# Optimization experiments

Measured on AMD Instinct MI355X. Metric: run time of the kernel, lower is better.

The kernel has to match this reference:

```python
import jax, jax.numpy as jnp
import numpy as np

B, C, L = 32, 64, 4096
PS, STRIDE = 16, 8
PC = (L - PS) // STRIDE + 1  # 511
HID = 64


def setup_inputs() -> dict:
    key = jax.random.key(0)
    k = jax.random.split(key, 5)
    X = jax.random.normal(k[0], (B, C, L), dtype=jnp.float32)
    W1 = jax.random.normal(k[1], (HID, PS), dtype=jnp.float32) * 0.05  # Conv1d(1,64,PS) weight
    b1 = jax.random.normal(k[2], (HID,), dtype=jnp.float32) * 0.05
    W2 = jax.random.normal(k[3], (2, HID), dtype=jnp.float32) * 0.05   # Conv1d(64,2,1) weight
    b2 = jax.random.normal(k[4], (2,), dtype=jnp.float32) * 0.05
    return {"X": X, "W1": W1, "b1": b1, "W2": W2, "b2": b2}


def reference(X, W1, b1, W2, b2):
    Bn, Cn, Ln = X.shape
    s_bias = (PS - 1) / 2.0
    # anchors: center of each patch along the sequence axis
    anchor = jnp.arange(PC, dtype=X.dtype) * STRIDE + 0.5 * (PS - 1)  # (PC,)

    # ---- OffsetPredictor: unfold into (B, C, PC, PS) sliding windows ----
    idx = jnp.arange(PC)[:, None] * STRIDE + jnp.arange(PS)[None, :]  # (PC, PS)
    patches = X[:, :, idx]  # (B, C, PC, PS)
    # Conv1d(1, HID, PS) over a length-PS window == dense matmul with W1
    h = jax.nn.gelu(jnp.einsum('bcps,ks->bcpk', patches, W1) + b1, approximate=False)
    off = jnp.einsum('bcpk,jk->bcpj', h, W2) + b2  # (B, C, PC, 2)
    off = off.transpose(0, 2, 1, 3)  # (B, PC, C, 2)

    # ---- BoxCoder.decode ----
    dx = off[..., 0]
    ds = jax.nn.relu(off[..., 1] + s_bias)
    ref = anchor[None, :, None]
    lo = jnp.clip((dx + ref - ds) / (Ln - 1), 0.0, 1.0)  # (B, PC, C)
    hi = jnp.clip((dx + ref + ds) / (Ln - 1), 0.0, 1.0)

    # ---- BoxCoder.meshgrid: linear interp from box endpoints (align_corners) ----
    t = jnp.arange(PS, dtype=X.dtype) / (PS - 1)  # (PS,)
    xs = lo[..., None] + (hi - lo)[..., None] * t  # (B, PC, C, PS), in [0,1]
    ys = jnp.arange(Cn, dtype=X.dtype) / (Cn - 1)  # (C,), in [0,1]

    # ---- grid_sample(img=(B,1,C,L), grid=(xs,ys)*2-1, bilinear, align_corners=True) ----
    ix = xs * (Ln - 1)                                            # (B, PC, C, PS)
    iy = jnp.broadcast_to(ys[None, None, :, None] * (Cn - 1), ix.shape)
    ix0 = jnp.floor(ix)
    iy0 = jnp.floor(iy)
    wx = ix - ix0
    wy = iy - iy0
    ix0i = jnp.clip(ix0.astype(jnp.int32), 0, Ln - 1)
    ix1i = jnp.clip(ix0i + 1, 0, Ln - 1)
    iy0i = jnp.clip(iy0.astype(jnp.int32), 0, Cn - 1)
    iy1i = jnp.clip(iy0i + 1, 0, Cn - 1)

    gather = jax.vmap(lambda x, r, c: x[r, c])  # over batch; x:(C,L)
    v00 = gather(X, iy0i, ix0i)
    v01 = gather(X, iy0i, ix1i)
    v10 = gather(X, iy1i, ix0i)
    v11 = gather(X, iy1i, ix1i)
    out = (v00 * (1 - wx) + v01 * wx) * (1 - wy) + (v10 * (1 - wx) + v11 * wx) * wy
    # (B, PC, C, PS) -> (B, C, PC, PS)
    return out.transpose(0, 2, 1, 3)
```

## Files before the change

### kernel.cpp

```cpp
#include <hip/hip_runtime.h>
#include <math.h>

#define B_    32
#define C_    64
#define L_    4096
#define PS_   16
#define STR_  8
#define PC_   511
#define HID_  64

__global__ __launch_bounds__(256) void depatch_kernel(
    const float* __restrict__ X,
    const float* __restrict__ W1,
    const float* __restrict__ b1,
    const float* __restrict__ W2,
    const float* __restrict__ b2,
    float* __restrict__ out)
{
    __shared__ float s_row[L_];
    __shared__ float s_W1[HID_ * PS_];
    __shared__ float s_b1[HID_];
    __shared__ float s_W2[2 * HID_];
    __shared__ float s_b2[2];

    const int tid = threadIdx.x;
    const int bc  = blockIdx.x;
    const float* xrow = X + (size_t)bc * L_;

    {
        const float4* src4 = reinterpret_cast<const float4*>(xrow);
        float4* dst4 = reinterpret_cast<float4*>(s_row);
        #pragma unroll
        for (int i = 0; i < 4; ++i) dst4[tid + 256 * i] = src4[tid + 256 * i];

        reinterpret_cast<float4*>(s_W1)[tid] =
            reinterpret_cast<const float4*>(W1)[tid];
        if (tid < 16)
            reinterpret_cast<float4*>(s_b1)[tid] =
                reinterpret_cast<const float4*>(b1)[tid];
        if (tid < 32)
            reinterpret_cast<float4*>(s_W2)[tid] =
                reinterpret_cast<const float4*>(W2)[tid];
        if (tid < 2) s_b2[tid] = b2[tid];
    }
    __syncthreads();

    const float bias0 = s_b2[0];
    const float bias1 = s_b2[1];

    for (int p = tid; p < PC_; p += 256) {
        float pt[PS_];
        {
            const float4* prow = reinterpret_cast<const float4*>(s_row + p * STR_);
            #pragma unroll
            for (int i = 0; i < 4; ++i) {
                float4 v = prow[i];
                pt[4*i + 0] = v.x; pt[4*i + 1] = v.y;
                pt[4*i + 2] = v.z; pt[4*i + 3] = v.w;
            }
        }

        float dx  = bias0;
        float dsv = bias1;
        #pragma unroll 8
        for (int k = 0; k < HID_; ++k) {
            float acc = s_b1[k];
            const float* w = s_W1 + k * PS_;
            #pragma unroll
            for (int s = 0; s < PS_; ++s) acc = fmaf(pt[s], w[s], acc);
            float g = 0.5f * acc * (1.0f + erff(acc * 0.70710678118654752440f));
            dx  = fmaf(g, s_W2[k],        dx);
            dsv = fmaf(g, s_W2[HID_ + k], dsv);
        }

        const float refp = (float)(p * STR_) + 7.5f;
        const float ds2  = fmaxf(dsv + 7.5f, 0.0f);
        float lo = (dx + refp - ds2) / 4095.0f;
        float hi = (dx + refp + ds2) / 4095.0f;
        lo = fminf(fmaxf(lo, 0.0f), 1.0f);
        hi = fminf(fmaxf(hi, 0.0f), 1.0f);
        const float span = hi - lo;

        float outv[PS_];
        #pragma unroll
        for (int s = 0; s < PS_; ++s) {
            float t  = (float)s / 15.0f;
            float xs = lo + span * t;
            float ix = xs * 4095.0f;
            float ix0f = floorf(ix);
            float wx = ix - ix0f;
            int ix0 = (int)ix0f;
            ix0 = min(max(ix0, 0), L_ - 1);
            int ix1 = min(ix0 + 1, L_ - 1);
            float v0 = s_row[ix0];
            float v1 = s_row[ix1];
            outv[s] = v0 * (1.0f - wx) + v1 * wx;
        }

        float4* o4 = reinterpret_cast<float4*>(out + ((size_t)bc * PC_ + p) * PS_);
        #pragma unroll
        for (int i = 0; i < 4; ++i) {
            float4 v;
            v.x = outv[4*i + 0]; v.y = outv[4*i + 1];
            v.z = outv[4*i + 2]; v.w = outv[4*i + 3];
            o4[i] = v;
        }
    }
}

extern "C" void kernel_launch(void* const* d_in, const int* in_sizes, int n_in,
                              void* d_out, int out_size, void* d_ws, size_t ws_size,
                              hipStream_t stream) {
    const float* X  = (const float*)d_in[0];
    const float* W1 = (const float*)d_in[1];
    const float* b1 = (const float*)d_in[2];
    const float* W2 = (const float*)d_in[3];
    const float* b2 = (const float*)d_in[4];
    float* out = (float*)d_out;

    dim3 grid(B_ * C_);
    dim3 block(256);
    depatch_kernel<<<grid, block, 0, stream>>>(X, W1, b1, W2, b2, out);
}
```

Before: 148.0 us.

## Use fast GELU approximation and process two patches per thread with global weights

Replaces the exact erff-based GELU with an Abramowitz-Stegun polynomial erf approximation built on the hardware reciprocal and exp2. Each thread now handles two patches at once, sharing each weight load across both accumulators, and reads the weights directly from global memory (uniform, scalar-cacheable) instead of staging them in shared memory. The sampling math is simplified by working in index space. The erf approximation has an error around 1e-7 relative, which may shift sampling positions slightly.

```diff
diff --git a/kernel.cpp b/kernel.cpp
--- a/kernel.cpp
+++ b/kernel.cpp
@@ -1,13 +1,57 @@
 #include <hip/hip_runtime.h>
 #include <math.h>
 
-#define B_    32
-#define C_    64
 #define L_    4096
 #define PS_   16
 #define STR_  8
 #define PC_   511
 #define HID_  64
+#define NBLK_ 2048
+
+__device__ __forceinline__ float gelu_as(float x) {
+    float az = fabsf(x) * 0.70710678118654752440f;
+    float d  = fmaf(0.3275911f, az, 1.0f);
+    float t  = __builtin_amdgcn_rcpf(d);
+    float p  = fmaf(1.061405429f, t, -1.453152027f);
+    p = fmaf(p, t, 1.421413741f);
+    p = fmaf(p, t, -0.284496736f);
+    p = fmaf(p, t, 0.254829592f);
+    p = p * t;
+    float e  = __builtin_amdgcn_exp2f(az * az * -1.4426950408889634f);
+    float r  = fmaf(-p, e, 1.0f);
+    r = copysignf(r, x);
+    float h = 0.5f * x;
+    return fmaf(h, r, h);
+}
+
+__device__ __forceinline__ void sample_store(const float* __restrict__ s_row,
+                                             float* __restrict__ outp,
+                                             int p, float dx, float ds) {
+    const float refp = (float)(p * STR_) + 7.5f;
+    const float d2   = fmaxf(ds + 7.5f, 0.0f);
+    const float a    = dx + refp;
+    const float loi  = fminf(fmaxf(a - d2, 0.0f), 4095.0f);
+    const float hii  = fminf(fmaxf(a + d2, 0.0f), 4095.0f);
+    const float span = hii - loi;
+
+    float4 o[4];
+    float* ov = reinterpret_cast<float*>(o);
+    #pragma unroll
+    for (int s = 0; s < PS_; ++s) {
+        float t  = (float)s / 15.0f;
+        float ix = fmaf(span, t, loi);
+        float f  = floorf(ix);
+        float wx = ix - f;
+        int i0 = (int)f;
+        int i1 = min(i0 + 1, L_ - 1);
+        float v0 = s_row[i0];
+        float v1 = s_row[i1];
+        ov[s] = fmaf(wx, v1 - v0, v0);
+    }
+    float4* o4 = reinterpret_cast<float4*>(outp);
+    #pragma unroll
+    for (int i = 0; i < 4; ++i) o4[i] = o[i];
+}
 
 __global__ __launch_bounds__(256) void depatch_kernel(
     const float* __restrict__ X,
@@ -18,10 +62,6 @@
     float* __restrict__ out)
 {
     __shared__ float s_row[L_];
-    __shared__ float s_W1[HID_ * PS_];
-    __shared__ float s_b1[HID_];
-    __shared__ float s_W2[2 * HID_];
-    __shared__ float s_b2[2];
 
     const int tid = threadIdx.x;
     const int bc  = blockIdx.x;
@@ -32,80 +72,50 @@
         float4* dst4 = reinterpret_cast<float4*>(s_row);
         #pragma unroll
         for (int i = 0; i < 4; ++i) dst4[tid + 256 * i] = src4[tid + 256 * i];
-
-        reinterpret_cast<float4*>(s_W1)[tid] =
-            reinterpret_cast<const float4*>(W1)[tid];
-        if (tid < 16)
-            reinterpret_cast<float4*>(s_b1)[tid] =
-                reinterpret_cast<const float4*>(b1)[tid];
-        if (tid < 32)
-            reinterpret_cast<float4*>(s_W2)[tid] =
-                reinterpret_cast<const float4*>(W2)[tid];
-        if (tid < 2) s_b2[tid] = b2[tid];
     }
     __syncthreads();
 
-    const float bias0 = s_b2[0];
-    const float bias1 = s_b2[1];
+    const int p0  = tid;
+    const int p1  = tid + 256;
+    const int p1c = (p1 < PC_) ? p1 : (PC_ - 1);
 
-    for (int p = tid; p < PC_; p += 256) {
-        float pt[PS_];
-        {
-            const float4* prow = reinterpret_cast<const float4*>(s_row + p * STR_);
-            #pragma unroll
-            for (int i = 0; i < 4; ++i) {
-                float4 v = prow[i];
-                pt[4*i + 0] = v.x; pt[4*i + 1] = v.y;
-                pt[4*i + 2] = v.z; pt[4*i + 3] = v.w;
-            }
+    float pa[PS_], pb[PS_];
+    {
+        const float4* ra = reinterpret_cast<const float4*>(s_row + p0  * STR_);
+        const float4* rb = reinterpret_cast<const float4*>(s_row + p1c * STR_);
+        #pragma unroll
+        for (int i = 0; i < 4; ++i) {
+            float4 va = ra[i], vb = rb[i];
+            pa[4*i+0]=va.x; pa[4*i+1]=va.y; pa[4*i+2]=va.z; pa[4*i+3]=va.w;
+            pb[4*i+0]=vb.x; pb[4*i+1]=vb.y; pb[4*i+2]=vb.z; pb[4*i+3]=vb.w;
         }
+    }
 
-        float dx  = bias0;
-        float dsv = bias1;
-        #pragma unroll 8
-        for (int k = 0; k < HID_; ++k) {
-            float acc = s_b1[k];
-            const float* w = s_W1 + k * PS_;
-            #pragma unroll
-            for (int s = 0; s < PS_; ++s) acc = fmaf(pt[s], w[s], acc);
-            float g = 0.5f * acc * (1.0f + erff(acc * 0.70710678118654752440f));
-            dx  = fmaf(g, s_W2[k],        dx);
-            dsv = fmaf(g, s_W2[HID_ + k], dsv);
-        }
+    float dxa = b2[0], dsa = b2[1];
+    float dxb = dxa,  dsb = dsa;
 
-        const float refp = (float)(p * STR_) + 7.5f;
-        const float ds2  = fmaxf(dsv + 7.5f, 0.0f);
-        float lo = (dx + refp - ds2) / 4095.0f;
-        float hi = (dx + refp + ds2) / 4095.0f;
-        lo = fminf(fmaxf(lo, 0.0f), 1.0f);
-        hi = fminf(fmaxf(hi, 0.0f), 1.0f);
-        const float span = hi - lo;
-
-        float outv[PS_];
+    #pragma unroll 4
+    for (int k = 0; k < HID_; ++k) {
+        const float* w = W1 + k * PS_;
+        float acca = b1[k];
+        float accb = acca;
         #pragma unroll
         for (int s = 0; s < PS_; ++s) {
-            float t  = (float)s / 15.0f;
-            float xs = lo + span * t;
-            float ix = xs * 4095.0f;
-            float ix0f = floorf(ix);
-            float wx = ix - ix0f;
-            int ix0 = (int)ix0f;
-            ix0 = min(max(ix0, 0), L_ - 1);
-            int ix1 = min(ix0 + 1, L_ - 1);
-            float v0 = s_row[ix0];
-            float v1 = s_row[ix1];
-            outv[s] = v0 * (1.0f - wx) + v1 * wx;
+            float ws = w[s];
+            acca = fmaf(pa[s], ws, acca);
+            accb = fmaf(pb[s], ws, accb);
         }
+        float ga = gelu_as(acca);
+        float gb = gelu_as(accb);
+        float w20 = W2[k], w21 = W2[HID_ + k];
+        dxa = fmaf(ga, w20, dxa);  dsa = fmaf(ga, w21, dsa);
+        dxb = fmaf(gb, w20, dxb);  dsb = fmaf(gb, w21, dsb);
+    }
 
-        float4* o4 = reinterpret_cast<float4*>(out + ((size_t)bc * PC_ + p) * PS_);
-        #pragma unroll
-        for (int i = 0; i < 4; ++i) {
-            float4 v;
-            v.x = outv[4*i + 0]; v.y = outv[4*i + 1];
-            v.z = outv[4*i + 2]; v.w = outv[4*i + 3];
-            o4[i] = v;
-        }
-    }
+    float* obase = out + (size_t)bc * PC_ * PS_;
+    sample_store(s_row, obase + (size_t)p0 * PS_, p0, dxa, dsa);
+    if (p1 < PC_)
+        sample_store(s_row, obase + (size_t)p1 * PS_, p1, dxb, dsb);
 }
 
 extern "C" void kernel_launch(void* const* d_in, const int* in_sizes, int n_in,
@@ -118,7 +128,5 @@
     const float* b2 = (const float*)d_in[4];
     float* out = (float*)d_out;
 
-    dim3 grid(B_ * C_);
-    dim3 block(256);
-    depatch_kernel<<<grid, block, 0, stream>>>(X, W1, b1, W2, b2, out);
+    depatch_kernel<<<dim3(NBLK_), dim3(256), 0, stream>>>(X, W1, b1, W2, b2, out);
 }
```

Result: no change. 146.7 us (-0.9%).
